# Kernel optimization log

Hardware: AMD Instinct MI355X
Metric: run time of the kernel (lower is better)

## Reference

```python
import jax, jax.numpy as jnp
import numpy as np

EPS = 1e-5

def channel_norm(x):
    # per-(batch,channel) norm over spatial dims; torch.var default is unbiased (ddof=1)
    mn = x.mean(axis=(-1, -2), keepdims=True)
    std = jnp.sqrt(x.var(axis=(-1, -2), keepdims=True, ddof=1) + EPS)
    return (x - mn) / std

def conv1x1(x, W, b):
    # x: [B,C,H,W], W: [O,C], b: [O]
    return jnp.einsum('oc,bchw->bohw', W, x) + b[None, :, None, None]

def setup_inputs() -> dict:
    key = jax.random.key(0)
    ks = jax.random.split(key, 10)
    B, C, H, W = 4, 512, 64, 64
    s = 1.0 / np.sqrt(C)  # kaiming-uniform-ish scale for 1x1 conv
    inp = {
        'f_c': jax.random.normal(ks[0], (B, C, H, W), jnp.float32),
        'f_s': jax.random.normal(ks[1], (B, C, H, W), jnp.float32),
        'W_c1': jax.random.uniform(ks[2], (C, C), jnp.float32, -s, s),
        'b_c1': jax.random.uniform(ks[3], (C,), jnp.float32, -s, s),
        'W_s1': jax.random.uniform(ks[4], (C, C), jnp.float32, -s, s),
        'b_s1': jax.random.uniform(ks[5], (C,), jnp.float32, -s, s),
        'W_s2': jax.random.uniform(ks[6], (C, C), jnp.float32, -s, s),
        'b_s2': jax.random.uniform(ks[7], (C,), jnp.float32, -s, s),
        'W_csc': jax.random.uniform(ks[8], (C, C), jnp.float32, -s, s),
        'b_csc': jax.random.uniform(ks[9], (C,), jnp.float32, -s, s),
    }
    return inp

def reference(f_c, f_s, W_c1, b_c1, W_s1, b_s1, W_s2, b_s2, W_csc, b_csc):
    B, C, H, W = f_c.shape
    f_c_hat = channel_norm(f_c)
    f_s_hat = channel_norm(f_s)
    f = conv1x1(f_c_hat, W_c1, b_c1).reshape(B, C, H * W)  # queries [B,C,N]
    g = conv1x1(f_s_hat, W_s1, b_s1).reshape(B, C, H * W)  # keys    [B,C,N]
    scores = jnp.einsum('bci,bcj->bij', f, g)              # [B,N,N]
    attention = jax.nn.softmax(scores, axis=-1)
    h = conv1x1(f_s_hat, W_s2, b_s2).reshape(B, C, H * W)  # values  [B,C,N]
    out = jnp.einsum('bcj,bij->bci', h, attention).reshape(B, C, H, W)
    return conv1x1(out, W_csc, b_csc) + f_c
```

## Files before the change

### kernel.cpp

```cpp
#include <hip/hip_runtime.h>

typedef unsigned short u16;
typedef __attribute__((ext_vector_type(8))) _Float16 f16x8;
typedef __attribute__((ext_vector_type(16))) float f32x16;

#define N_SP 4096
#define C_CH 512
#define B_SZ 4

struct PtrTab { u16* p[4]; };

__device__ __forceinline__ u16 f2h(float f) {
    union { _Float16 h; u16 u; } x; x.h = (_Float16)f; return x.u;
}
__device__ __forceinline__ float h2f(u16 u) {
    union { u16 u; _Float16 h; } x; x.u = u; return (float)x.h;
}
__device__ __forceinline__ void async_cp16(const void* g, void* l) {
    __builtin_amdgcn_global_load_lds((const __attribute__((address_space(1))) unsigned*)g,
                                     (__attribute__((address_space(3))) unsigned*)l, 16, 0, 0);
}
__device__ __forceinline__ float wave_reduce_sum(float v) {
    #pragma unroll
    for (int off = 32; off; off >>= 1) v += __shfl_xor(v, off, 64);
    return v;
}
__device__ __forceinline__ float wave_reduce_max(float v) {
    #pragma unroll
    for (int off = 32; off; off >>= 1) v = fmaxf(v, __shfl_xor(v, off, 64));
    return v;
}
__device__ __forceinline__ void bar() { asm volatile("s_barrier" ::: "memory"); }
template<int N> __device__ __forceinline__ void vmwait() {
    if constexpr (N == 0)  asm volatile("s_waitcnt vmcnt(0)" ::: "memory");
    else if constexpr (N == 2)  asm volatile("s_waitcnt vmcnt(2)" ::: "memory");
    else if constexpr (N == 3)  asm volatile("s_waitcnt vmcnt(3)" ::: "memory");
    else if constexpr (N == 4)  asm volatile("s_waitcnt vmcnt(4)" ::: "memory");
    else if constexpr (N == 6)  asm volatile("s_waitcnt vmcnt(6)" ::: "memory");
    else if constexpr (N == 8)  asm volatile("s_waitcnt vmcnt(8)" ::: "memory");
}

__global__ __launch_bounds__(256) void transpose_cast_stats(
        const float* __restrict__ fc, const float* __restrict__ fs,
        u16* __restrict__ xc, u16* __restrict__ xs,
        float* __restrict__ part_s, float* __restrict__ part_ss) {
    __shared__ float tile[64][65];
    const int t = threadIdx.x;
    const int n0 = blockIdx.x * 64, c0 = blockIdx.y * 64;
    const int z = blockIdx.z;
    const int b = z & 3, which = z >> 2;
    const float* src = which ? fs : fc;
    u16* dst = which ? xs : xc;
    const int r = t >> 4, q4 = (t & 15) * 4;
    #pragma unroll
    for (int it = 0; it < 4; ++it) {
        const int row = it * 16 + r;
        float4 v = *(const float4*)(src + ((size_t)b * C_CH + c0 + row) * N_SP + n0 + q4);
        tile[row][q4 + 0] = v.x; tile[row][q4 + 1] = v.y;
        tile[row][q4 + 2] = v.z; tile[row][q4 + 3] = v.w;
    }
    __syncthreads();
    {
        const int cr = t >> 2, q = t & 3;
        float s = 0.f, ss = 0.f;
        #pragma unroll
        for (int i = 0; i < 16; ++i) {
            float a = tile[cr][q * 16 + i];
            s += a; ss += a * a;
        }
        s += __shfl_xor(s, 1, 64);  s += __shfl_xor(s, 2, 64);
        ss += __shfl_xor(ss, 1, 64); ss += __shfl_xor(ss, 2, 64);
        if (q == 0) {
            atomicAdd(&part_s[z * 512 + c0 + cr], s);
            atomicAdd(&part_ss[z * 512 + c0 + cr], ss);
        }
    }
    #pragma unroll
    for (int it = 0; it < 4; ++it) {
        const int nrow = it * 16 + r;
        ushort4 h4;
        h4.x = f2h(tile[q4 + 0][nrow]);
        h4.y = f2h(tile[q4 + 1][nrow]);
        h4.z = f2h(tile[q4 + 2][nrow]);
        h4.w = f2h(tile[q4 + 3][nrow]);
        *(ushort4*)(dst + ((size_t)b * N_SP + n0 + nrow) * C_CH + c0 + q4) = h4;
    }
}

__global__ __launch_bounds__(256) void prep1(
        const float* __restrict__ W_c1, const float* __restrict__ W_s1,
        const float* __restrict__ W_s2, const float* __restrict__ W_csc,
        const float* __restrict__ b_c1, const float* __restrict__ b_s2,
        const float* __restrict__ b_csc,
        u16* __restrict__ Wbase,
        const float* __restrict__ part_s, const float* __restrict__ part_ss,
        float* __restrict__ mu_a, float* __restrict__ rs_a,
        float* __restrict__ w_u, float* __restrict__ bfold0) {
    __shared__ float tile[64][65];
    const int t = threadIdx.x, z = blockIdx.z;
    if (z < 4) {
        const int n0 = blockIdx.x * 64, c0 = blockIdx.y * 64;
        const float* W = (z == 0) ? W_c1 : (z == 1) ? W_s1 : (z == 2) ? W_s2 : W_csc;
        u16* D = Wbase + ((z == 0) ? 2 : (z == 1) ? 0 : (z == 2) ? 3 : 1) * 262144;
        const int r = t >> 4, q4 = (t & 15) * 4;
        #pragma unroll
        for (int it = 0; it < 4; ++it) {
            const int row = it * 16 + r;
            float4 v = *(const float4*)(W + (size_t)(c0 + row) * 512 + n0 + q4);
            if (z == 3) {
                ushort4 h4 = { f2h(v.x), f2h(v.y), f2h(v.z), f2h(v.w) };
                *(ushort4*)(D + (size_t)(c0 + row) * 512 + n0 + q4) = h4;
            } else {
                tile[row][q4 + 0] = v.x; tile[row][q4 + 1] = v.y;
                tile[row][q4 + 2] = v.z; tile[row][q4 + 3] = v.w;
            }
        }
        __syncthreads();
        if (z == 3) return;
        #pragma unroll
        for (int it = 0; it < 4; ++it) {
            const int nrow = it * 16 + r;
            ushort4 h4;
            h4.x = f2h(tile[q4 + 0][nrow]);
            h4.y = f2h(tile[q4 + 1][nrow]);
            h4.z = f2h(tile[q4 + 2][nrow]);
            h4.w = f2h(tile[q4 + 3][nrow]);
            *(ushort4*)(D + (size_t)(n0 + nrow) * 512 + c0 + q4) = h4;
        }
        return;
    }
    const int flat = blockIdx.y * 8 + blockIdx.x;
    if (flat < 8) {
        #pragma unroll
        for (int h = 0; h < 2; ++h) {
            const int c = flat * 512 + h * 256 + t;
            const float S = part_s[c], SS = part_ss[c];
            const float mean = S * (1.f / N_SP);
            const float var = (SS - S * mean) * (1.f / (N_SP - 1));
            mu_a[c] = mean;
            rs_a[c] = rsqrtf(var + 1e-5f);
        }
    } else if (flat < 10) {
        const int d = (flat - 8) * 256 + t;
        float acc = 0.f;
        for (int o = 0; o < 512; ++o) acc += b_c1[o] * W_s1[(size_t)o * 512 + d];
        w_u[d] = acc;
    } else if (flat < 42) {
        const int w4 = t >> 6, l = t & 63;
        #pragma unroll
        for (int q = 0; q < 4; ++q) {
            const int o = (flat - 10) * 16 + w4 * 4 + q;
            const float4 w0 = *(const float4*)(W_csc + (size_t)o * 512 + l * 8);
            const float4 w1 = *(const float4*)(W_csc + (size_t)o * 512 + l * 8 + 4);
            const float4 b0 = *(const float4*)(b_s2 + l * 8);
            const float4 b1 = *(const float4*)(b_s2 + l * 8 + 4);
            float acc = w0.x * b0.x + w0.y * b0.y + w0.z * b0.z + w0.w * b0.w
                      + w1.x * b1.x + w1.y * b1.y + w1.z * b1.z + w1.w * b1.w;
            acc = wave_reduce_sum(acc);
            if (l == 0) bfold0[o] = acc + b_csc[o];
        }
    }
}

__global__ __launch_bounds__(256) void prep2(
        const u16* __restrict__ WqT16, const u16* __restrict__ Wf16,
        const u16* __restrict__ xs,
        const float* __restrict__ mu_a, const float* __restrict__ rs_a,
        const float* __restrict__ bfold0, const float* __restrict__ w_u,
        u16* __restrict__ Wq_z, u16* __restrict__ Wf_z,
        float* __restrict__ bq, float* __restrict__ bh, float* __restrict__ u_) {
    const int id = blockIdx.x, t = threadIdx.x;
    if (id < 1024) {
        const int y = id >> 9;
        const size_t e = ((size_t)(id & 511) * 256 + t) * 8;
        const int z = (int)(e >> 18), rem = (int)(e & 262143);
        const int d = rem >> 9, a0 = rem & 511;
        u16 v[8];
        if (y == 0) {
            *(uint4*)v = *(const uint4*)(WqT16 + rem);
            const float rd = rs_a[(4 + z) * 512 + d];
            const float* rc = rs_a + z * 512 + a0;
            #pragma unroll
            for (int i = 0; i < 8; ++i) v[i] = f2h(h2f(v[i]) * rc[i] * rd);
            *(uint4*)(Wq_z + e) = *(const uint4*)v;
        } else {
            *(uint4*)v = *(const uint4*)(Wf16 + rem);
            const float* rk = rs_a + (4 + z) * 512 + a0;
            #pragma unroll
            for (int i = 0; i < 8; ++i) v[i] = f2h(h2f(v[i]) * rk[i]);
            *(uint4*)(Wf_z + e) = *(const uint4*)v;
        }
    } else if (id < 2048) {
        const int w = t >> 6, l = t & 63;
        const int oid = (id - 1024) * 4 + w;
        const int kind = oid >> 11;
        const int z = (oid >> 9) & 3, d = oid & 511;
        const u16* row = (kind == 0 ? WqT16 : Wf16) + (size_t)d * 512;
        const int sb = (kind == 0 ? z : 4 + z) * 512;
        float acc = 0.f;
        #pragma unroll
        for (int i = 0; i < 8; ++i) {
            const int a = l * 8 + i;
            acc += h2f(row[a]) * mu_a[sb + a] * rs_a[sb + a];
        }
        acc = wave_reduce_sum(acc);
        if (l == 0) {
            if (kind == 0) bq[z * 512 + d] = -acc * rs_a[(4 + z) * 512 + d];
            else           bh[z * 512 + d] = bfold0[d] - acc;
        }
    } else {
        const int id2 = id - 2048;
        const int b = id2 >> 6, xblk = id2 & 63;
        const int w = t >> 6, l = t & 63;
        float4 u0 = *(const float4*)(w_u + l * 8);
        float4 u1 = *(const float4*)(w_u + l * 8 + 4);
        const float4 r0 = *(const float4*)(rs_a + (4 + b) * 512 + l * 8);
        const float4 r1 = *(const float4*)(rs_a + (4 + b) * 512 + l * 8 + 4);
        u0.x *= r0.x; u0.y *= r0.y; u0.z *= r0.z; u0.w *= r0.w;
        u1.x *= r1.x; u1.y *= r1.y; u1.z *= r1.z; u1.w *= r1.w;
        #pragma unroll
        for (int jj = 0; jj < 16; ++jj) {
            const int j = xblk * 64 + w * 16 + jj;
            const u16* row = xs + ((size_t)b * N_SP + j) * C_CH + l * 8;
            f16x8 x = *(const f16x8*)row;
            float acc = (float)x[0] * u0.x + (float)x[1] * u0.y + (float)x[2] * u0.z + (float)x[3] * u0.w
                      + (float)x[4] * u1.x + (float)x[5] * u1.y + (float)x[6] * u1.z + (float)x[7] * u1.w;
            acc = wave_reduce_sum(acc);
            if (l == 0) u_[(size_t)b * N_SP + j] = acc;
        }
    }
}

enum { OUT_F32 = 0, OUT_F16 = 1 };

template<int OUTMODE, bool TABB, bool TABD, int MI, int MJ>
__global__ __launch_bounds__(256) void gemm_bt(
    const u16* __restrict__ A, const u16* __restrict__ B, PtrTab tab,
    float* __restrict__ Df, u16* __restrict__ Dh,
    const float* __restrict__ bias_m, const float* __restrict__ bias_n,
    const float* __restrict__ res,
    int M, int N, int K, int lda, int ldb, int ldd,
    size_t sA, size_t sB, size_t sD, size_t sR, int sBm, int sBn)
{
    constexpr int TM = MI * 64, TN = MJ * 64, BK = 64;
    constexpr int AITS = (TM * BK) / (256 * 8);
    constexpr int BITS = (TN * BK) / (256 * 8);
    __shared__ u16 smem[(TM + TN) * BK];
    u16* As = smem;
    u16* Bs = smem + TM * BK;

    const int t = threadIdx.x;
    const int l = t & 63, w = t >> 6;
    const int m0 = blockIdx.y * TM, n0 = blockIdx.x * TN;
    const size_t zb = blockIdx.z;
    const u16* pA = A + zb * sA + (size_t)m0 * lda;
    const u16* pB = (TABB ? tab.p[zb] : B + zb * sB) + (size_t)n0 * ldb;

    const int wr = (w & 1) * (MI * 32), wc = (w >> 1) * (MJ * 32);

    f32x16 acc[MI][MJ] = {};

    for (int k0 = 0; k0 < K; k0 += BK) {
        #pragma unroll
        for (int it = 0; it < AITS; ++it) {
            const int L = it * 256 + t;
            const int row = L >> 3, c = L & 7;
            const int sc = (c ^ (row & 7)) * 8;
            async_cp16(pA + (size_t)row * lda + k0 + sc, As + L * 8);
        }
        #pragma unroll
        for (int it = 0; it < BITS; ++it) {
            const int L = it * 256 + t;
            const int row = L >> 3, c = L & 7;
            const int sc = (c ^ (row & 7)) * 8;
            async_cp16(pB + (size_t)row * ldb + k0 + sc, Bs + L * 8);
        }
        __syncthreads();
        #pragma unroll
        for (int kk = 0; kk < 4; ++kk) {
            f16x8 af[MI], bf[MJ];
            #pragma unroll
            for (int i = 0; i < MI; ++i) {
                const int row = wr + i * 32 + (l & 31);
                const int ch = ((kk * 2 + (l >> 5)) ^ (row & 7)) * 8;
                af[i] = *(const f16x8*)(As + row * BK + ch);
            }
            #pragma unroll
            for (int j = 0; j < MJ; ++j) {
                const int row = wc + j * 32 + (l & 31);
                const int ch = ((kk * 2 + (l >> 5)) ^ (row & 7)) * 8;
                bf[j] = *(const f16x8*)(Bs + row * BK + ch);
            }
            #pragma unroll
            for (int i = 0; i < MI; ++i)
                #pragma unroll
                for (int j = 0; j < MJ; ++j)
                    acc[i][j] = __builtin_amdgcn_mfma_f32_32x32x16_f16(af[i], bf[j], acc[i][j], 0, 0, 0);
        }
        __syncthreads();
    }

    const int cl = l & 31, rh = (l >> 5) * 4;
    u16* pDh = (OUTMODE == OUT_F16) ? (TABD ? tab.p[zb] : Dh + zb * sD) : nullptr;
    float* pDf = (OUTMODE == OUT_F32) ? (Df + zb * sD) : nullptr;
    #pragma unroll
    for (int i = 0; i < MI; ++i) {
        #pragma unroll
        for (int j = 0; j < MJ; ++j) {
            const int nn = n0 + wc + j * 32 + cl;
            const float bn = bias_n ? bias_n[(size_t)sBn * zb + nn] : 0.f;
            #pragma unroll
            for (int reg = 0; reg < 16; ++reg) {
                const int ml = (reg & 3) + 8 * (reg >> 2) + rh;
                const int mm = m0 + wr + i * 32 + ml;
                float v = acc[i][j][reg] + bn;
                if (bias_m) v += bias_m[(size_t)sBm * zb + mm];
                const size_t off = (size_t)mm * ldd + nn;
                if (OUTMODE == OUT_F32) {
                    if (res) v += res[zb * sR + off];
                    pDf[off] = v;
                } else {
                    pDh[off] = f2h(v);
                }
            }
        }
    }
}

template<int OUTMODE, bool TABB, bool TABD, int BM, int BN>
__global__ __launch_bounds__(512, 2) void gemm_p8(
    const u16* __restrict__ A, const u16* __restrict__ B, PtrTab tab,
    float* __restrict__ Df, u16* __restrict__ Dh,
    const float* __restrict__ bias_m, const float* __restrict__ bias_n,
    const float* __restrict__ res,
    int K, int lda, int ldb, int ldd,
    size_t sA, size_t sB, size_t sD, size_t sR, int sBm, int sBn)
{
    constexpr int BK = 64;
    constexpr int LDSH = (BM + BN) * BK;
    constexpr int MI_Q = BM / 128;
    constexpr int LA = BM / 128, LB = BN / 128;
    constexpr int WN = LA + LB;
    static_assert(BN == 256, "col mapping assumes BN=256");
    __shared__ u16 smem[2 * LDSH];

    const int t = threadIdx.x;
    const int l = t & 63, w = t >> 6;

    const int gx = gridDim.x, nxy = gx * gridDim.y;
    const int orig = blockIdx.x + gx * blockIdx.y;
    const int wg = (orig & 7) * (nxy >> 3) + (orig >> 3);
    const int m0 = (wg / gx) * BM, n0 = (wg % gx) * BN;

    const size_t zb = blockIdx.z;
    const u16* pA = A + zb * sA + (size_t)m0 * lda;
    const u16* pB = (TABB ? tab.p[zb] : B + zb * sB) + (size_t)n0 * ldb;

    f32x16 acc[2][2][MI_Q] = {};

    auto stageA = [&](int buf, int k0, int rh) {
        u16* dst = smem + buf * LDSH;
        #pragma unroll
        for (int it = 0; it < LA; ++it) {
            const int L = it * 512 + t;
            const int row = rh * (BM / 2) + (L >> 3), c = L & 7;
            const int sc = (c ^ (row & 7)) * 8;
            async_cp16(pA + (size_t)row * lda + k0 + sc, dst + row * BK + c * 8);
        }
    };
    auto stageB = [&](int buf, int k0, int rh) {
        u16* dst = smem + buf * LDSH + BM * BK;
        #pragma unroll
        for (int it = 0; it < LB; ++it) {
            const int L = it * 512 + t;
            const int row = rh * (BN / 2) + (L >> 3), c = L & 7;
            const int sc = (c ^ (row & 7)) * 8;
            async_cp16(pB + (size_t)row * ldb + k0 + sc, dst + row * BK + c * 8);
        }
    };

    const int NT = K / BK;
    stageA(0, 0, 0); stageB(0, 0, 0); stageA(0, 0, 1); stageB(0, 0, 1);
    vmwait<WN>();
    bar();

    for (int tl = 0; tl < NT; ++tl) {
        const int cur = tl & 1, nxt = cur ^ 1;
        const u16* As = smem + cur * LDSH;
        const u16* Bs = As + BM * BK;
        const int k1 = (tl + 1) * BK;
        const bool pf = (tl + 1 < NT);

        #pragma unroll
        for (int ph = 0; ph < 4; ++ph) {
            constexpr int QI[4] = {0, 1, 1, 0};
            constexpr int QJ[4] = {0, 0, 1, 1};
            const int qi = QI[ph], qj = QJ[ph];
            const int rbase = qi * (BM / 2) + (w & 1) * (BM / 4);
            const int cbase = qj * (BN / 2) + (w >> 1) * (BN / 8);

            f16x8 af[MI_Q][4], bf[4];
            #pragma unroll
            for (int fi = 0; fi < MI_Q; ++fi)
                #pragma unroll
                for (int kk = 0; kk < 4; ++kk) {
                    const int row = rbase + fi * 32 + (l & 31);
                    const int ch = ((kk * 2 + (l >> 5)) ^ (row & 7)) * 8;
                    af[fi][kk] = *(const f16x8*)(As + row * BK + ch);
                }
            #pragma unroll
            for (int kk = 0; kk < 4; ++kk) {
                const int row = cbase + (l & 31);
                const int ch = ((kk * 2 + (l >> 5)) ^ (row & 7)) * 8;
                bf[kk] = *(const f16x8*)(Bs + row * BK + ch);
            }

            if (pf) {
                if      (ph == 0) stageA(nxt, k1, 0);
                else if (ph == 1) stageB(nxt, k1, 0);
                else if (ph == 2) stageA(nxt, k1, 1);
                else              stageB(nxt, k1, 1);
            }
            if (ph == 0) { if (pf) vmwait<WN>(); else vmwait<0>(); }
            else if ((ph == 1 || ph == 3) && pf) vmwait<WN>();

            bar();
            asm volatile("s_waitcnt lgkmcnt(0)" ::: "memory");
            __builtin_amdgcn_sched_barrier(0);
            __builtin_amdgcn_s_setprio(1);
            #pragma unroll
            for (int fi = 0; fi < MI_Q; ++fi)
                #pragma unroll
                for (int kk = 0; kk < 4; ++kk)
                    acc[qi][qj][fi] = __builtin_amdgcn_mfma_f32_32x32x16_f16(
                        af[fi][kk], bf[kk], acc[qi][qj][fi], 0, 0, 0);
            __builtin_amdgcn_s_setprio(0);
            bar();
        }
    }

    const int cl = l & 31, rhh = (l >> 5) * 4;
    u16* pDh = (OUTMODE == OUT_F16) ? (TABD ? tab.p[zb] : Dh + zb * sD) : nullptr;
    float* pDf = (OUTMODE == OUT_F32) ? (Df + zb * sD) : nullptr;
    #pragma unroll
    for (int qi = 0; qi < 2; ++qi) {
        #pragma unroll
        for (int qj = 0; qj < 2; ++qj) {
            #pragma unroll
            for (int fi = 0; fi < MI_Q; ++fi) {
                const int nn = n0 + qj * (BN / 2) + (w >> 1) * (BN / 8) + cl;
                const float bn = bias_n ? bias_n[(size_t)sBn * zb + nn] : 0.f;
                #pragma unroll
                for (int reg = 0; reg < 16; ++reg) {
                    const int ml = (reg & 3) + 8 * (reg >> 2) + rhh;
                    const int mm = m0 + qi * (BM / 2) + (w & 1) * (BM / 4) + fi * 32 + ml;
                    float v = acc[qi][qj][fi][reg] + bn;
                    if (bias_m) v += bias_m[(size_t)sBm * zb + mm];
                    const size_t off = (size_t)mm * ldd + nn;
                    if (OUTMODE == OUT_F32) {
                        if (res) v += res[zb * sR + off];
                        pDf[off] = v;
                    } else {
                        pDh[off] = f2h(v);
                    }
                }
            }
        }
    }
}

__global__ __launch_bounds__(256) void softmax_kernel(PtrTab tab) {
    u16* row = tab.p[blockIdx.y] + (size_t)blockIdx.x * N_SP;
    const int t = threadIdx.x;
    u16 raw[16];
    *(uint4*)(raw + 0) = *(const uint4*)(row + t * 16);
    *(uint4*)(raw + 8) = *(const uint4*)(row + t * 16 + 8);
    float v[16];
    float mx = -1e30f;
    #pragma unroll
    for (int i = 0; i < 16; ++i) { v[i] = h2f(raw[i]); mx = fmaxf(mx, v[i]); }
    mx = wave_reduce_max(mx);
    __shared__ float red[4];
    const int wave = t >> 6;
    if ((t & 63) == 0) red[wave] = mx;
    __syncthreads();
    mx = fmaxf(fmaxf(red[0], red[1]), fmaxf(red[2], red[3]));
    float sum = 0.f;
    #pragma unroll
    for (int i = 0; i < 16; ++i) { v[i] = __expf(v[i] - mx); sum += v[i]; }
    sum = wave_reduce_sum(sum);
    __syncthreads();
    if ((t & 63) == 0) red[wave] = sum;
    __syncthreads();
    const float inv = 1.f / (red[0] + red[1] + red[2] + red[3]);
    #pragma unroll
    for (int i = 0; i < 16; ++i) raw[i] = f2h(v[i] * inv);
    *(uint4*)(row + t * 16)     = *(const uint4*)(raw + 0);
    *(uint4*)(row + t * 16 + 8) = *(const uint4*)(raw + 8);
}

extern "C" void kernel_launch(void* const* d_in, const int* in_sizes, int n_in,
                              void* d_out, int out_size, void* d_ws, size_t ws_size,
                              hipStream_t stream) {
    const float* f_c   = (const float*)d_in[0];
    const float* f_s   = (const float*)d_in[1];
    const float* W_c1  = (const float*)d_in[2];
    const float* b_c1  = (const float*)d_in[3];
    const float* W_s1  = (const float*)d_in[4];
    const float* b_s1  = (const float*)d_in[5]; (void)b_s1;
    const float* W_s2  = (const float*)d_in[6];
    const float* b_s2  = (const float*)d_in[7];
    const float* W_csc = (const float*)d_in[8];
    const float* b_csc = (const float*)d_in[9];

    const size_t PB = (size_t)N_SP * C_CH;
    const size_t M1 = 1024 * 1024;

    u16* ws   = (u16*)d_ws;
    u16* Xs   = ws;
    u16* q_   = ws + 8 * M1;
    u16* hc   = ws + 16 * M1;
    u16* Xc   = ws + 24 * M1;
    u16* S3   = ws + 24 * M1;
    u16* S0   = ws + 40 * M1;
    u16* S1   = ws + 56 * M1;
    u16* S2   = ws + 72 * M1;
    u16* Wbase= ws + 88 * M1;
    u16* WqT16= Wbase + 4 * 262144;
    u16* Wf16 = Wbase + 5 * 262144;
    u16* Wq_z = Wbase + 6 * 262144;
    u16* Wf_z = Wq_z + 1048576;
    float* f32b = (float*)(ws + 92 * M1);
    float* part_s  = f32b;
    float* part_ss = f32b + 4096;
    float* mu_a    = f32b + 8192;
    float* rs_a    = f32b + 12288;
    float* w_u     = f32b + 16384;
    float* bfold0  = f32b + 16896;
    float* bq      = f32b + 17408;
    float* bh      = f32b + 19456;
    float* u_      = f32b + 21504;

    PtrTab Stab; Stab.p[0] = S0; Stab.p[1] = S1; Stab.p[2] = S2; Stab.p[3] = S3;
    PtrTab tab0 = Stab;

    hipMemsetAsync(part_s, 0, 2 * 4096 * sizeof(float), stream);

    transpose_cast_stats<<<dim3(64, 8, 8), 256, 0, stream>>>(f_c, f_s, Xc, Xs, part_s, part_ss);

    prep1<<<dim3(8, 8, 5), 256, 0, stream>>>(W_c1, W_s1, W_s2, W_csc, b_c1, b_s2, b_csc,
                                             Wbase, part_s, part_ss, mu_a, rs_a, w_u, bfold0);

    gemm_bt<OUT_F16, false, false, 2, 2><<<dim3(4, 4, 2), 256, 0, stream>>>(
        Wbase, Wbase + 2 * 262144, tab0, nullptr, WqT16, nullptr, nullptr, nullptr,
        512, 512, 512, 512, 512, 512, 262144, 262144, 262144, 0, 0, 0);

    prep2<<<2304, 256, 0, stream>>>(WqT16, Wf16, Xs, mu_a, rs_a, bfold0, w_u,
                                    Wq_z, Wf_z, bq, bh, u_);

    gemm_p8<OUT_F16, false, false, 128, 256><<<dim3(2, 32, B_SZ), 512, 0, stream>>>(
        Xc, Wq_z, tab0, nullptr, q_, nullptr, bq, nullptr,
        C_CH, C_CH, C_CH, C_CH, PB, 262144, PB, 0, 0, 512);
    gemm_p8<OUT_F16, false, false, 128, 256><<<dim3(16, 4, B_SZ), 512, 0, stream>>>(
        Wf_z, Xs, tab0, nullptr, hc, bh, nullptr, nullptr,
        C_CH, C_CH, C_CH, N_SP, 262144, PB, PB, 0, 512, 0);

    gemm_p8<OUT_F16, false, true, 256, 256><<<dim3(16, 16, B_SZ), 512, 0, stream>>>(
        q_, Xs, Stab, nullptr, nullptr, nullptr, u_, nullptr,
        C_CH, C_CH, C_CH, N_SP, PB, PB, 0, 0, 0, N_SP);

    softmax_kernel<<<dim3(N_SP, B_SZ), 256, 0, stream>>>(Stab);

    gemm_p8<OUT_F32, true, false, 128, 256><<<dim3(16, 4, B_SZ), 512, 0, stream>>>(
        hc, nullptr, Stab, (float*)d_out, nullptr, nullptr, nullptr, f_c,
        N_SP, N_SP, N_SP, N_SP, PB, 0, PB, PB, 0, 0);
}
```

Before: 475.5 us.

## Rewrite GEMM main loop with 16x16x32 MFMA and register fragment reuse

Replaces the 32x32x16 MFMA GEMM with a variant built on 16x16x32 MFMA tiles. A and B fragments are carried across quadrant phases so each LDS fragment load serves two quadrants, with a new XOR swizzle that matches the 16-lane read pattern. It also drops the XCD-aware workgroup remapping in favour of plain blockIdx tile indexing. This aims to cut LDS read traffic and sync overhead, but risks worse L2 locality without the remap and lower per-instruction MFMA efficiency from the smaller tiles.

```diff
diff --git a/kernel.cpp b/kernel.cpp
--- a/kernel.cpp
+++ b/kernel.cpp
@@ -2,6 +2,7 @@
 
 typedef unsigned short u16;
 typedef __attribute__((ext_vector_type(8))) _Float16 f16x8;
+typedef __attribute__((ext_vector_type(4))) float f32x4;
 typedef __attribute__((ext_vector_type(16))) float f32x16;
 
 #define N_SP 4096
@@ -327,8 +328,8 @@
     }
 }
 
-template<int OUTMODE, bool TABB, bool TABD, int BM, int BN>
-__global__ __launch_bounds__(512, 2) void gemm_p8(
+template<int OUTMODE, bool TABB, bool TABD, int BM>
+__global__ __launch_bounds__(512, 2) void gemm_p16(
     const u16* __restrict__ A, const u16* __restrict__ B, PtrTab tab,
     float* __restrict__ Df, u16* __restrict__ Dh,
     const float* __restrict__ bias_m, const float* __restrict__ bias_n,
@@ -336,53 +337,61 @@
     int K, int lda, int ldb, int ldd,
     size_t sA, size_t sB, size_t sD, size_t sR, int sBm, int sBn)
 {
-    constexpr int BK = 64;
+    constexpr int BN = 256, BK = 64;
+    constexpr int HM = BM / 2;
+    constexpr int MF = BM / 64;
+    constexpr int LA = BM / 128;
+    constexpr int LB = 2;
     constexpr int LDSH = (BM + BN) * BK;
-    constexpr int MI_Q = BM / 128;
-    constexpr int LA = BM / 128, LB = BN / 128;
-    constexpr int WN = LA + LB;
-    static_assert(BN == 256, "col mapping assumes BN=256");
     __shared__ u16 smem[2 * LDSH];
 
     const int t = threadIdx.x;
     const int l = t & 63, w = t >> 6;
-
-    const int gx = gridDim.x, nxy = gx * gridDim.y;
-    const int orig = blockIdx.x + gx * blockIdx.y;
-    const int wg = (orig & 7) * (nxy >> 3) + (orig >> 3);
-    const int m0 = (wg / gx) * BM, n0 = (wg % gx) * BN;
-
+    const int m0 = blockIdx.y * BM, n0 = blockIdx.x * BN;
     const size_t zb = blockIdx.z;
     const u16* pA = A + zb * sA + (size_t)m0 * lda;
     const u16* pB = (TABB ? tab.p[zb] : B + zb * sB) + (size_t)n0 * ldb;
 
-    f32x16 acc[2][2][MI_Q] = {};
-
-    auto stageA = [&](int buf, int k0, int rh) {
+    const int wr = (w & 1) * (HM / 2);
+    const int wc = (w >> 1) * 32;
+
+    f32x4 acc[2 * MF][4] = {};
+
+    auto stageA = [&](int buf, int k0, int half) {
         u16* dst = smem + buf * LDSH;
         #pragma unroll
         for (int it = 0; it < LA; ++it) {
             const int L = it * 512 + t;
-            const int row = rh * (BM / 2) + (L >> 3), c = L & 7;
-            const int sc = (c ^ (row & 7)) * 8;
-            async_cp16(pA + (size_t)row * lda + k0 + sc, dst + row * BK + c * 8);
+            const int row = half * HM + (L >> 3), c = L & 7;
+            const int cs = c ^ (((row >> 2) & 1) << 1);
+            async_cp16(pA + (size_t)row * lda + k0 + cs * 8, dst + row * BK + c * 8);
         }
     };
-    auto stageB = [&](int buf, int k0, int rh) {
+    auto stageB = [&](int buf, int k0, int half) {
         u16* dst = smem + buf * LDSH + BM * BK;
         #pragma unroll
         for (int it = 0; it < LB; ++it) {
             const int L = it * 512 + t;
-            const int row = rh * (BN / 2) + (L >> 3), c = L & 7;
-            const int sc = (c ^ (row & 7)) * 8;
-            async_cp16(pB + (size_t)row * ldb + k0 + sc, dst + row * BK + c * 8);
-        }
+            const int row = half * 128 + (L >> 3), c = L & 7;
+            const int cs = c ^ (((row >> 2) & 1) << 1);
+            async_cp16(pB + (size_t)row * ldb + k0 + cs * 8, dst + row * BK + c * 8);
+        }
+    };
+    auto rdA = [&](const u16* As, int qi, int mf, int kk) -> f16x8 {
+        const int row = qi * HM + wr + mf * 16 + (l & 15);
+        const int ch = (kk * 4 + (l >> 4)) ^ (((row >> 2) & 1) << 1);
+        return *(const f16x8*)(As + row * BK + ch * 8);
+    };
+    auto rdB = [&](const u16* Bs, int qj, int nf, int kk) -> f16x8 {
+        const int row = qj * 128 + wc + nf * 16 + (l & 15);
+        const int ch = (kk * 4 + (l >> 4)) ^ (((row >> 2) & 1) << 1);
+        return *(const f16x8*)(Bs + row * BK + ch * 8);
     };
 
     const int NT = K / BK;
     stageA(0, 0, 0); stageB(0, 0, 0); stageA(0, 0, 1); stageB(0, 0, 1);
-    vmwait<WN>();
-    bar();
+
+    f16x8 af[MF][2], bf[2][2];
 
     for (int tl = 0; tl < NT; ++tl) {
         const int cur = tl & 1, nxt = cur ^ 1;
@@ -391,55 +400,87 @@
         const int k1 = (tl + 1) * BK;
         const bool pf = (tl + 1 < NT);
 
-        #pragma unroll
-        for (int ph = 0; ph < 4; ++ph) {
-            constexpr int QI[4] = {0, 1, 1, 0};
-            constexpr int QJ[4] = {0, 0, 1, 1};
-            const int qi = QI[ph], qj = QJ[ph];
-            const int rbase = qi * (BM / 2) + (w & 1) * (BM / 4);
-            const int cbase = qj * (BN / 2) + (w >> 1) * (BN / 8);
-
-            f16x8 af[MI_Q][4], bf[4];
-            #pragma unroll
-            for (int fi = 0; fi < MI_Q; ++fi)
-                #pragma unroll
-                for (int kk = 0; kk < 4; ++kk) {
-                    const int row = rbase + fi * 32 + (l & 31);
-                    const int ch = ((kk * 2 + (l >> 5)) ^ (row & 7)) * 8;
-                    af[fi][kk] = *(const f16x8*)(As + row * BK + ch);
-                }
-            #pragma unroll
-            for (int kk = 0; kk < 4; ++kk) {
-                const int row = cbase + (l & 31);
-                const int ch = ((kk * 2 + (l >> 5)) ^ (row & 7)) * 8;
-                bf[kk] = *(const f16x8*)(Bs + row * BK + ch);
-            }
-
-            if (pf) {
-                if      (ph == 0) stageA(nxt, k1, 0);
-                else if (ph == 1) stageB(nxt, k1, 0);
-                else if (ph == 2) stageA(nxt, k1, 1);
-                else              stageB(nxt, k1, 1);
-            }
-            if (ph == 0) { if (pf) vmwait<WN>(); else vmwait<0>(); }
-            else if ((ph == 1 || ph == 3) && pf) vmwait<WN>();
-
-            bar();
-            asm volatile("s_waitcnt lgkmcnt(0)" ::: "memory");
-            __builtin_amdgcn_sched_barrier(0);
-            __builtin_amdgcn_s_setprio(1);
-            #pragma unroll
-            for (int fi = 0; fi < MI_Q; ++fi)
-                #pragma unroll
-                for (int kk = 0; kk < 4; ++kk)
-                    acc[qi][qj][fi] = __builtin_amdgcn_mfma_f32_32x32x16_f16(
-                        af[fi][kk], bf[kk], acc[qi][qj][fi], 0, 0, 0);
-            __builtin_amdgcn_s_setprio(0);
-            bar();
-        }
-    }
-
-    const int cl = l & 31, rhh = (l >> 5) * 4;
+        vmwait<LA + LB>();
+        bar();
+        #pragma unroll
+        for (int mf = 0; mf < MF; ++mf) {
+            af[mf][0] = rdA(As, 0, mf, 0); af[mf][1] = rdA(As, 0, mf, 1);
+        }
+        #pragma unroll
+        for (int nf = 0; nf < 2; ++nf) {
+            bf[nf][0] = rdB(Bs, 0, nf, 0); bf[nf][1] = rdB(Bs, 0, nf, 1);
+        }
+        if (pf) stageA(nxt, k1, 0);
+        asm volatile("s_waitcnt lgkmcnt(0)" ::: "memory");
+        __builtin_amdgcn_sched_barrier(0);
+        __builtin_amdgcn_s_setprio(1);
+        #pragma unroll
+        for (int mf = 0; mf < MF; ++mf)
+            #pragma unroll
+            for (int nf = 0; nf < 2; ++nf) {
+                acc[mf][nf] = __builtin_amdgcn_mfma_f32_16x16x32_f16(af[mf][0], bf[nf][0], acc[mf][nf], 0, 0, 0);
+                acc[mf][nf] = __builtin_amdgcn_mfma_f32_16x16x32_f16(af[mf][1], bf[nf][1], acc[mf][nf], 0, 0, 0);
+            }
+        __builtin_amdgcn_s_setprio(0);
+
+        if (pf) vmwait<LA + LB>(); else vmwait<LB>();
+        bar();
+        #pragma unroll
+        for (int mf = 0; mf < MF; ++mf) {
+            af[mf][0] = rdA(As, 1, mf, 0); af[mf][1] = rdA(As, 1, mf, 1);
+        }
+        if (pf) stageB(nxt, k1, 0);
+        asm volatile("s_waitcnt lgkmcnt(0)" ::: "memory");
+        __builtin_amdgcn_sched_barrier(0);
+        __builtin_amdgcn_s_setprio(1);
+        #pragma unroll
+        for (int mf = 0; mf < MF; ++mf)
+            #pragma unroll
+            for (int nf = 0; nf < 2; ++nf) {
+                acc[MF + mf][nf] = __builtin_amdgcn_mfma_f32_16x16x32_f16(af[mf][0], bf[nf][0], acc[MF + mf][nf], 0, 0, 0);
+                acc[MF + mf][nf] = __builtin_amdgcn_mfma_f32_16x16x32_f16(af[mf][1], bf[nf][1], acc[MF + mf][nf], 0, 0, 0);
+            }
+        __builtin_amdgcn_s_setprio(0);
+
+        if (pf) vmwait<LA + LB>(); else vmwait<0>();
+        bar();
+        #pragma unroll
+        for (int nf = 0; nf < 2; ++nf) {
+            bf[nf][0] = rdB(Bs, 1, nf, 0); bf[nf][1] = rdB(Bs, 1, nf, 1);
+        }
+        if (pf) stageA(nxt, k1, 1);
+        asm volatile("s_waitcnt lgkmcnt(0)" ::: "memory");
+        __builtin_amdgcn_sched_barrier(0);
+        __builtin_amdgcn_s_setprio(1);
+        #pragma unroll
+        for (int mf = 0; mf < MF; ++mf)
+            #pragma unroll
+            for (int nf = 0; nf < 2; ++nf) {
+                acc[MF + mf][2 + nf] = __builtin_amdgcn_mfma_f32_16x16x32_f16(af[mf][0], bf[nf][0], acc[MF + mf][2 + nf], 0, 0, 0);
+                acc[MF + mf][2 + nf] = __builtin_amdgcn_mfma_f32_16x16x32_f16(af[mf][1], bf[nf][1], acc[MF + mf][2 + nf], 0, 0, 0);
+            }
+        __builtin_amdgcn_s_setprio(0);
+
+        bar();
+        #pragma unroll
+        for (int mf = 0; mf < MF; ++mf) {
+            af[mf][0] = rdA(As, 0, mf, 0); af[mf][1] = rdA(As, 0, mf, 1);
+        }
+        if (pf) stageB(nxt, k1, 1);
+        asm volatile("s_waitcnt lgkmcnt(0)" ::: "memory");
+        __builtin_amdgcn_sched_barrier(0);
+        __builtin_amdgcn_s_setprio(1);
+        #pragma unroll
+        for (int mf = 0; mf < MF; ++mf)
+            #pragma unroll
+            for (int nf = 0; nf < 2; ++nf) {
+                acc[mf][2 + nf] = __builtin_amdgcn_mfma_f32_16x16x32_f16(af[mf][0], bf[nf][0], acc[mf][2 + nf], 0, 0, 0);
+                acc[mf][2 + nf] = __builtin_amdgcn_mfma_f32_16x16x32_f16(af[mf][1], bf[nf][1], acc[mf][2 + nf], 0, 0, 0);
+            }
+        __builtin_amdgcn_s_setprio(0);
+    }
+
+    const int cl = l & 15, rh = (l >> 4) * 4;
     u16* pDh = (OUTMODE == OUT_F16) ? (TABD ? tab.p[zb] : Dh + zb * sD) : nullptr;
     float* pDf = (OUTMODE == OUT_F32) ? (Df + zb * sD) : nullptr;
     #pragma unroll
@@ -447,21 +488,24 @@
         #pragma unroll
         for (int qj = 0; qj < 2; ++qj) {
             #pragma unroll
-            for (int fi = 0; fi < MI_Q; ++fi) {
-                const int nn = n0 + qj * (BN / 2) + (w >> 1) * (BN / 8) + cl;
-                const float bn = bias_n ? bias_n[(size_t)sBn * zb + nn] : 0.f;
+            for (int mf = 0; mf < MF; ++mf) {
                 #pragma unroll
-                for (int reg = 0; reg < 16; ++reg) {
-                    const int ml = (reg & 3) + 8 * (reg >> 2) + rhh;
-                    const int mm = m0 + qi * (BM / 2) + (w & 1) * (BM / 4) + fi * 32 + ml;
-                    float v = acc[qi][qj][fi][reg] + bn;
-                    if (bias_m) v += bias_m[(size_t)sBm * zb + mm];
-                    const size_t off = (size_t)mm * ldd + nn;
-                    if (OUTMODE == OUT_F32) {
-                        if (res) v += res[zb * sR + off];
-                        pDf[off] = v;
-                    } else {
-                        pDh[off] = f2h(v);
+                for (int nf = 0; nf < 2; ++nf) {
+                    const int nn = n0 + qj * 128 + wc + nf * 16 + cl;
+                    const float bn = bias_n ? bias_n[(size_t)sBn * zb + nn] : 0.f;
+                    const f32x4 a4 = acc[qi * MF + mf][qj * 2 + nf];
+                    #pragma unroll
+                    for (int reg = 0; reg < 4; ++reg) {
+                        const int mm = m0 + qi * HM + wr + mf * 16 + rh + reg;
+                        float v = a4[reg] + bn;
+                        if (bias_m) v += bias_m[(size_t)sBm * zb + mm];
+                        const size_t off = (size_t)mm * ldd + nn;
+                        if (OUTMODE == OUT_F32) {
+                            if (res) v += res[zb * sR + off];
+                            pDf[off] = v;
+                        } else {
+                            pDh[off] = f2h(v);
+                        }
                     }
                 }
             }
@@ -558,20 +602,20 @@
     prep2<<<2304, 256, 0, stream>>>(WqT16, Wf16, Xs, mu_a, rs_a, bfold0, w_u,
                                     Wq_z, Wf_z, bq, bh, u_);
 
-    gemm_p8<OUT_F16, false, false, 128, 256><<<dim3(2, 32, B_SZ), 512, 0, stream>>>(
+    gemm_p16<OUT_F16, false, false, 128><<<dim3(2, 32, B_SZ), 512, 0, stream>>>(
         Xc, Wq_z, tab0, nullptr, q_, nullptr, bq, nullptr,
         C_CH, C_CH, C_CH, C_CH, PB, 262144, PB, 0, 0, 512);
-    gemm_p8<OUT_F16, false, false, 128, 256><<<dim3(16, 4, B_SZ), 512, 0, stream>>>(
+    gemm_p16<OUT_F16, false, false, 128><<<dim3(16, 4, B_SZ), 512, 0, stream>>>(
         Wf_z, Xs, tab0, nullptr, hc, bh, nullptr, nullptr,
         C_CH, C_CH, C_CH, N_SP, 262144, PB, PB, 0, 512, 0);
 
-    gemm_p8<OUT_F16, false, true, 256, 256><<<dim3(16, 16, B_SZ), 512, 0, stream>>>(
+    gemm_p16<OUT_F16, false, true, 256><<<dim3(16, 16, B_SZ), 512, 0, stream>>>(
         q_, Xs, Stab, nullptr, nullptr, nullptr, u_, nullptr,
         C_CH, C_CH, C_CH, N_SP, PB, PB, 0, 0, 0, N_SP);
 
     softmax_kernel<<<dim3(N_SP, B_SZ), 256, 0, stream>>>(Stab);
 
-    gemm_p8<OUT_F32, true, false, 128, 256><<<dim3(16, 4, B_SZ), 512, 0, stream>>>(
+    gemm_p16<OUT_F32, true, false, 128><<<dim3(16, 4, B_SZ), 512, 0, stream>>>(
         hc, nullptr, Stab, (float*)d_out, nullptr, nullptr, nullptr, f_c,
         N_SP, N_SP, N_SP, N_SP, PB, 0, PB, PB, 0, 0);
 }
```

Result: faster. 446.1 us (-6.2%).
